# Kernel optimization log

Measured on AMD Instinct MI355X. Metric: run time of the kernel, lower is better.

The kernel has to match this reference:

```python
import jax, jax.numpy as jnp
import numpy as np

A = -0.75  # torch bicubic 'a' coefficient


def _cubic_conv_w(t):
    # Keys cubic-convolution weights for taps at offsets -1,0,1,2; t in [0,1). -> [4, out]
    offs = jnp.arange(-1.0, 3.0, dtype=jnp.float32)
    d = jnp.abs(t[None, :] - offs[:, None])
    w_near = ((A + 2.0) * d - (A + 3.0)) * d * d + 1.0
    w_far = A * (((d - 5.0) * d + 8.0) * d - 4.0)
    return jnp.where(d <= 1.0, w_near, jnp.where(d < 2.0, w_far, 0.0))


def _resize_last(x, out_size):
    # torch F.interpolate(mode='bicubic', align_corners=False) along last axis, replicate border
    in_size = x.shape[-1]
    scale = in_size / out_size
    pos = (jnp.arange(out_size, dtype=jnp.float32) + 0.5) * scale - 0.5
    i0 = jnp.floor(pos)
    t = pos - i0
    offs = jnp.arange(-1, 3)
    idx = jnp.clip(i0.astype(jnp.int32)[None, :] + offs[:, None], 0, in_size - 1)  # [4, out]
    w = _cubic_conv_w(t)  # [4, out]
    taps = x[..., idx]  # [..., 4, out]
    return (taps * w).sum(-2)


def bicubic_resize(x, out_h, out_w):
    x = _resize_last(x, out_w)
    x = jnp.swapaxes(_resize_last(jnp.swapaxes(x, -1, -2), out_h), -1, -2)
    return x


def _bspline3_w(f):
    # cubic B-spline basis weights at taps floor-1..floor+2, f = frac in [0,1)
    f2 = f * f
    f3 = f2 * f
    w0 = (1.0 - 3.0 * f + 3.0 * f2 - f3) / 6.0
    w1 = (4.0 - 6.0 * f2 + 3.0 * f3) / 6.0
    w2 = (1.0 + 3.0 * f + 3.0 * f2 - 3.0 * f3) / 6.0
    w3 = f3 / 6.0
    return (w0, w1, w2, w3)


def grid_pull_cubic(img, grid):
    # img: [N, C, H, W] spline coefficients; grid: [H, W, 2] voxel coords (shared over batch)
    # bound='nearest' (replicate clamp), extrapolate=1 (no out-of-bound masking)
    H, W = img.shape[-2:]
    gy, gx = grid[..., 0], grid[..., 1]
    fy, fx = jnp.floor(gy), jnp.floor(gx)
    wy = _bspline3_w(gy - fy)
    wx = _bspline3_w(gx - fx)
    iy = [jnp.clip(fy.astype(jnp.int32) + k - 1, 0, H - 1) for k in range(4)]
    ix = [jnp.clip(fx.astype(jnp.int32) + k - 1, 0, W - 1) for k in range(4)]
    out = jnp.zeros(img.shape[:-2] + gy.shape, img.dtype)
    for i in range(4):
        row = jnp.zeros_like(out)
        for j in range(4):
            row = row + wx[j] * img[..., iy[i], ix[j]]  # gather -> [N, C, H, W]
        out = out + wy[i] * row
    return out


def setup_inputs() -> dict:
    key = jax.random.key(0)
    k1, k2 = jax.random.split(key)
    image_coordinates = jax.random.uniform(k1, (16, 1024, 1024, 2), jnp.float32)
    displacements = jax.random.normal(k2, (16, 2, 32, 32), jnp.float32) * 0.05
    return {"image_coordinates": image_coordinates, "displacements": displacements}


def reference(image_coordinates, displacements):
    N, H, W, _ = image_coordinates.shape
    # bicubic upsample of coarse control-point displacements to image resolution
    up = bicubic_resize(displacements, H, W)  # [N, 2, H, W]
    # identity grid in voxel coordinates (registered buffer in the torch module)
    yy, xx = jnp.meshgrid(jnp.arange(H, dtype=jnp.float32),
                          jnp.arange(W, dtype=jnp.float32), indexing='ij')
    grid = jnp.stack([yy, xx], axis=-1)  # [H, W, 2]
    deltas = grid_pull_cubic(up, grid)  # [N, 2, H, W]
    return image_coordinates + jnp.moveaxis(deltas, 1, -1)
```

## Files before the change

kernel.cpp:

```cpp
#include <hip/hip_runtime.h>


#define A_COEF (-0.75f)

__device__ __forceinline__ float wnear(float d) {
    return ((A_COEF + 2.0f) * d - (A_COEF + 3.0f)) * d * d + 1.0f;
}
__device__ __forceinline__ float wfar(float d) {
    return A_COEF * (((d - 5.0f) * d + 8.0f) * d - 4.0f);
}

__device__ __forceinline__ void combined_weights(int q, float* w, int* s_out) {
    float acc[5] = {0.f, 0.f, 0.f, 0.f, 0.f};
    const float inv32 = 1.0f / 32.0f;

    int ym = max(q - 1, 0);
    float posm = ((float)ym + 0.5f) * inv32 - 0.5f;
    int i0min = (int)floorf(posm);
    int s = i0min - 1;

#pragma unroll
    for (int dy = -1; dy <= 1; ++dy) {
        float b = (dy == 0) ? (2.0f / 3.0f) : (1.0f / 6.0f);
        int yp = min(max(q + dy, 0), 1023);
        float pos = ((float)yp + 0.5f) * inv32 - 0.5f;
        float fi = floorf(pos);
        int i0 = (int)fi;
        float t = pos - fi;
        float w4_0 = wfar(1.0f + t);
        float w4_1 = wnear(t);
        float w4_2 = wnear(1.0f - t);
        float w4_3 = wfar(2.0f - t);
        int off = i0 - i0min;
        float w4[4] = {w4_0, w4_1, w4_2, w4_3};
#pragma unroll
        for (int m = 0; m < 5; ++m) {
            float c0 = (m < 4) ? w4[m] : 0.0f;
            float c1 = (m >= 1) ? w4[m - 1] : 0.0f;
            acc[m] += b * ((off == 0) ? c0 : c1);
        }
    }
#pragma unroll
    for (int m = 0; m < 5; ++m) w[m] = acc[m];
    *s_out = s;
}

__global__ __launch_bounds__(256) void bsw_kernel(
    const float* __restrict__ coords,
    const float* __restrict__ disp,
    float* __restrict__ out)
{
    __shared__ __align__(16) float Dl[2][32][32];
    __shared__ float wyl[32][5];
    __shared__ int   syl[32];

    const int b   = blockIdx.x;
    const int n   = b >> 7;
    const int r   = b & 127;
    const int ty  = r >> 2;
    const int tx  = r & 3;
    const int y0  = ty << 5;
    const int x0  = tx << 8;
    const int tid = threadIdx.x;

    {
        const float4* dsrc = (const float4*)(disp + (size_t)n * 2048);
        float4* ddst = (float4*)(&Dl[0][0][0]);
        ddst[tid]       = dsrc[tid];
        ddst[tid + 256] = dsrc[tid + 256];
    }

    if (tid < 32) {
        float w[5]; int s;
        combined_weights(y0 + tid, w, &s);
#pragma unroll
        for (int m = 0; m < 5; ++m) wyl[tid][m] = w[m];
        syl[tid] = s;
    }

    const int x = x0 + tid;
    float wx[5]; int sx;
    combined_weights(x, wx, &sx);
    int cx[5];
#pragma unroll
    for (int j = 0; j < 5; ++j) cx[j] = min(max(sx + j, 0), 31);

    __syncthreads();

    const int s0 = syl[0];

    float T0[6], T1[6];
#pragma unroll
    for (int k = 0; k < 6; ++k) {
        int rk = min(max(s0 + k, 0), 31);
        float a0 = 0.f, a1 = 0.f;
#pragma unroll
        for (int j = 0; j < 5; ++j) {
            a0 += wx[j] * Dl[0][rk][cx[j]];
            a1 += wx[j] * Dl[1][rk][cx[j]];
        }
        T0[k] = a0; T1[k] = a1;
    }

    const size_t base = ((size_t)n << 20) + ((size_t)y0 << 10) + (size_t)x;
    const float2* cp = (const float2*)coords + base;
    float2* op = (float2*)out + base;

#pragma unroll 4
    for (int yi = 0; yi < 32; ++yi) {
        const int shift = syl[yi] - s0;
        float wy[5];
#pragma unroll
        for (int m = 0; m < 5; ++m) wy[m] = wyl[yi][m];
        float w6[6];
#pragma unroll
        for (int k = 0; k < 6; ++k) {
            float a0 = (k < 5) ? wy[k] : 0.0f;
            float a1 = (k >= 1) ? wy[k - 1] : 0.0f;
            w6[k] = (shift == 0) ? a0 : a1;
        }
        float d0 = 0.f, d1 = 0.f;
#pragma unroll
        for (int k = 0; k < 6; ++k) {
            d0 += w6[k] * T0[k];
            d1 += w6[k] * T1[k];
        }
        float2 c = cp[(size_t)yi << 10];
        float2 o;
        o.x = c.x + d0;
        o.y = c.y + d1;
        op[(size_t)yi << 10] = o;
    }
}

extern "C" void kernel_launch(void* const* d_in, const int* in_sizes, int n_in,
                              void* d_out, int out_size, void* d_ws, size_t ws_size,
                              hipStream_t stream) {
    const float* coords = (const float*)d_in[0];
    const float* disp   = (const float*)d_in[1];
    float* out = (float*)d_out;

    bsw_kernel<<<2048, 256, 0, stream>>>(coords, disp, out);
}
```

Baseline: 50.65 us.

## Process two pixels per thread with 16-byte loads and nontemporal stores

Each thread now handles two adjacent x pixels, so coordinate loads and output stores become 128-bit vectors. Block tiles change from 32x256 to 16x512, which halves the rows per block. Output stores use nontemporal hints to avoid polluting the cache. The cost is extra per-thread weight computation and more registers, and the coarse-row shift assumption now holds over 16 rows.

```diff
diff --git a/kernel.cpp b/kernel.cpp
--- a/kernel.cpp
+++ b/kernel.cpp
@@ -1,5 +1,7 @@
 #include <hip/hip_runtime.h>
 
+
+typedef float f32x4 __attribute__((ext_vector_type(4)));
 
 #define A_COEF (-0.75f)
 
@@ -51,26 +53,26 @@
     float* __restrict__ out)
 {
     __shared__ __align__(16) float Dl[2][32][32];
-    __shared__ float wyl[32][5];
-    __shared__ int   syl[32];
+    __shared__ float wyl[16][5];
+    __shared__ int   syl[16];
 
     const int b   = blockIdx.x;
     const int n   = b >> 7;
     const int r   = b & 127;
-    const int ty  = r >> 2;
-    const int tx  = r & 3;
-    const int y0  = ty << 5;
-    const int x0  = tx << 8;
+    const int ty  = r >> 1;
+    const int tx  = r & 1;
+    const int y0  = ty << 4;
+    const int x0  = tx << 9;
     const int tid = threadIdx.x;
 
     {
-        const float4* dsrc = (const float4*)(disp + (size_t)n * 2048);
-        float4* ddst = (float4*)(&Dl[0][0][0]);
+        const f32x4* dsrc = (const f32x4*)(disp + (size_t)n * 2048);
+        f32x4* ddst = (f32x4*)(&Dl[0][0][0]);
         ddst[tid]       = dsrc[tid];
         ddst[tid + 256] = dsrc[tid + 256];
     }
 
-    if (tid < 32) {
+    if (tid < 16) {
         float w[5]; int s;
         combined_weights(y0 + tid, w, &s);
 #pragma unroll
@@ -78,36 +80,42 @@
         syl[tid] = s;
     }
 
-    const int x = x0 + tid;
-    float wx[5]; int sx;
-    combined_weights(x, wx, &sx);
-    int cx[5];
+    const int xa = x0 + (tid << 1);
+    float wxa[5], wxb[5]; int sxa, sxb;
+    combined_weights(xa, wxa, &sxa);
+    combined_weights(xa + 1, wxb, &sxb);
+    int cxa[5], cxb[5];
 #pragma unroll
-    for (int j = 0; j < 5; ++j) cx[j] = min(max(sx + j, 0), 31);
+    for (int j = 0; j < 5; ++j) {
+        cxa[j] = min(max(sxa + j, 0), 31);
+        cxb[j] = min(max(sxb + j, 0), 31);
+    }
 
     __syncthreads();
 
     const int s0 = syl[0];
 
-    float T0[6], T1[6];
+    float Ta0[6], Ta1[6], Tb0[6], Tb1[6];
 #pragma unroll
     for (int k = 0; k < 6; ++k) {
         int rk = min(max(s0 + k, 0), 31);
-        float a0 = 0.f, a1 = 0.f;
+        float a0 = 0.f, a1 = 0.f, b0 = 0.f, b1 = 0.f;
 #pragma unroll
         for (int j = 0; j < 5; ++j) {
-            a0 += wx[j] * Dl[0][rk][cx[j]];
-            a1 += wx[j] * Dl[1][rk][cx[j]];
+            a0 += wxa[j] * Dl[0][rk][cxa[j]];
+            a1 += wxa[j] * Dl[1][rk][cxa[j]];
+            b0 += wxb[j] * Dl[0][rk][cxb[j]];
+            b1 += wxb[j] * Dl[1][rk][cxb[j]];
         }
-        T0[k] = a0; T1[k] = a1;
+        Ta0[k] = a0; Ta1[k] = a1; Tb0[k] = b0; Tb1[k] = b1;
     }
 
-    const size_t base = ((size_t)n << 20) + ((size_t)y0 << 10) + (size_t)x;
-    const float2* cp = (const float2*)coords + base;
-    float2* op = (float2*)out + base;
+    const size_t base4 = ((size_t)n << 19) + ((size_t)y0 << 9) + (size_t)(x0 >> 1) + (size_t)tid;
+    const f32x4* cp = (const f32x4*)coords + base4;
+    f32x4* op = (f32x4*)out + base4;
 
 #pragma unroll 4
-    for (int yi = 0; yi < 32; ++yi) {
+    for (int yi = 0; yi < 16; ++yi) {
         const int shift = syl[yi] - s0;
         float wy[5];
 #pragma unroll
@@ -119,17 +127,21 @@
             float a1 = (k >= 1) ? wy[k - 1] : 0.0f;
             w6[k] = (shift == 0) ? a0 : a1;
         }
-        float d0 = 0.f, d1 = 0.f;
+        float da0 = 0.f, da1 = 0.f, db0 = 0.f, db1 = 0.f;
 #pragma unroll
         for (int k = 0; k < 6; ++k) {
-            d0 += w6[k] * T0[k];
-            d1 += w6[k] * T1[k];
+            da0 += w6[k] * Ta0[k];
+            da1 += w6[k] * Ta1[k];
+            db0 += w6[k] * Tb0[k];
+            db1 += w6[k] * Tb1[k];
         }
-        float2 c = cp[(size_t)yi << 10];
-        float2 o;
-        o.x = c.x + d0;
-        o.y = c.y + d1;
-        op[(size_t)yi << 10] = o;
+        f32x4 c = cp[(size_t)yi << 9];
+        f32x4 o;
+        o.x = c.x + da0;
+        o.y = c.y + da1;
+        o.z = c.z + db0;
+        o.w = c.w + db1;
+        __builtin_nontemporal_store(o, &op[(size_t)yi << 9]);
     }
 }
 
```

Measured after the change: 46.73 us. -7.7%, faster.
